# Optimization experiments

Measured on AMD Instinct MI355X. Metric: run time of the kernel, lower is better.

## Reference

```python
import jax, jax.numpy as jnp
import numpy as np

B, S, HID = 1, 4096, 2048
NH, NKV, HD = 8, 4, 256
SCALING = 256.0 ** -0.5
SOFT_CAP = 50.0
WINDOW = 4096
ROPE_THETA = 10000.0
NEG = jnp.finfo(jnp.float32).min


def _build_mask():
    q = np.arange(S)[:, None]
    k = np.arange(S)[None, :]
    causal = k <= q
    windowed = (q - k) < WINDOW
    allowed = causal & windowed
    m = np.where(allowed, 0.0, np.finfo(np.float32).min).astype(np.float32)
    return jnp.asarray(m)[None, None]  # [1,1,S,S]


def setup_inputs() -> dict:
    key = jax.random.key(0)
    ks = jax.random.split(key, 5)
    scale = 0.02
    return {
        "hidden_states": jax.random.normal(ks[0], (B, S, HID), jnp.float32),
        "attention_mask": _build_mask(),
        "position_ids": jnp.arange(S, dtype=jnp.int64)[None, :],
        "wq": jax.random.normal(ks[1], (HID, NH * HD), jnp.float32) * scale,
        "wk": jax.random.normal(ks[2], (HID, NKV * HD), jnp.float32) * scale,
        "wv": jax.random.normal(ks[3], (HID, NKV * HD), jnp.float32) * scale,
        "wo": jax.random.normal(ks[4], (NH * HD, HID), jnp.float32) * scale,
    }


def _rope(position_ids):
    inv_freq = 1.0 / (ROPE_THETA ** (jnp.arange(0, HD, 2, dtype=jnp.float32) / HD))
    freqs = position_ids.astype(jnp.float32)[:, :, None] * inv_freq[None, None, :]  # [B,S,HD/2]
    emb = jnp.concatenate([freqs, freqs], axis=-1)  # [B,S,HD]
    return jnp.cos(emb), jnp.sin(emb)


def _rotate_half(x):
    x1, x2 = x[..., : HD // 2], x[..., HD // 2 :]
    return jnp.concatenate([-x2, x1], axis=-1)


def _attn(hidden_states, attention_mask, position_ids, wq, wk, wv, wo):
    bsz, q_len, _ = hidden_states.shape
    q = (hidden_states @ wq).reshape(bsz, q_len, NH, HD).transpose(0, 2, 1, 3)    # [B,NH,S,HD]
    k = (hidden_states @ wk).reshape(bsz, q_len, NKV, HD).transpose(0, 2, 1, 3)   # [B,NKV,S,HD]
    v = (hidden_states @ wv).reshape(bsz, q_len, NKV, HD).transpose(0, 2, 1, 3)
    cos, sin = _rope(position_ids)
    cos, sin = cos[:, None], sin[:, None]  # [B,1,S,HD]
    q = q * cos + _rotate_half(q) * sin
    k = k * cos + _rotate_half(k) * sin
    n_rep = NH // NKV
    k = jnp.repeat(k, n_rep, axis=1)  # [B,NH,S,HD]
    v = jnp.repeat(v, n_rep, axis=1)
    scores = jnp.einsum("bhqd,bhkd->bhqk", q, k) * SCALING
    scores = jnp.tanh(scores / SOFT_CAP) * SOFT_CAP
    scores = scores + attention_mask
    probs = jax.nn.softmax(scores.astype(jnp.float32), axis=-1).astype(q.dtype)
    out = jnp.einsum("bhqk,bhkd->bhqd", probs, v)  # [B,NH,S,HD]
    out = out.transpose(0, 2, 1, 3).reshape(bsz, q_len, NH * HD)
    return out @ wo


def reference(hidden_states, attention_mask, position_ids, wq, wk, wv, wo):
    return _attn(hidden_states, attention_mask, position_ids, wq, wk, wv, wo)
```

## Files before the change

### kernel.cpp

```cpp
#include <hip/hip_runtime.h>


#define SEQ 4096
#define HIDDEN 2048
#define NHEADS 8
#define HDIM 256

typedef unsigned short u16;
typedef __attribute__((ext_vector_type(8))) __bf16 bf16x8;
typedef __attribute__((ext_vector_type(4))) float f32x4;
typedef __attribute__((ext_vector_type(16))) float f32x16;

static __device__ inline u16 f2bf(float f) {
  union { float f; unsigned u; } x; x.f = f;
  unsigned r = x.u + 0x7FFFu + ((x.u >> 16) & 1u);
  return (u16)(r >> 16);
}
static __device__ inline float bf2f(u16 u) {
  union { unsigned u; float f; } x; x.u = ((unsigned)u) << 16;
  return x.f;
}

typedef __attribute__((address_space(1))) const unsigned int* gp_t;
typedef __attribute__((address_space(3))) unsigned int* lp_t;
static __device__ inline void load_lds16(const u16* g, u16* l) {
  __builtin_amdgcn_global_load_lds((gp_t)g, (lp_t)l, 16, 0, 0);
}


__global__ void convert_hs_kernel(const float* __restrict__ src, u16* __restrict__ dst) {
  int i = blockIdx.x * 256 + threadIdx.x;
  float4 v = ((const float4*)src)[i];
  ushort4 o;
  o.x = f2bf(v.x); o.y = f2bf(v.y); o.z = f2bf(v.z); o.w = f2bf(v.w);
  ((ushort4*)dst)[i] = o;
}

__global__ void transpose_w_kernel(const float* __restrict__ src, u16* __restrict__ dst,
                                   int K, int N) {
  __shared__ u16 tile[64][65];
  int n0 = blockIdx.x * 64, k0 = blockIdx.y * 64;
  int tid = threadIdx.x;
  for (int i = 0; i < 16; i++) {
    int idx = i * 256 + tid; int r = idx >> 6, c = idx & 63;
    tile[r][c] = f2bf(src[(size_t)(k0 + r) * N + n0 + c]);
  }
  __syncthreads();
  for (int i = 0; i < 16; i++) {
    int idx = i * 256 + tid; int r = idx >> 6, c = idx & 63;
    dst[(size_t)(n0 + r) * K + k0 + c] = tile[c][r];
  }
}

__global__ void rope_kernel(u16* qkv) {
  int idx = blockIdx.x * 256 + threadIdx.x;
  int s = idx / (12 * 128);
  int rem = idx - s * (12 * 128);
  int head = rem >> 7;
  int i = rem & 127;
  float inv = __expf(-(float)i * 0.0719557841560639f);
  float ang = (float)s * inv;
  float sn, cs;
  sincosf(ang, &sn, &cs);
  size_t base = (size_t)s * 4096 + head * 256 + i;
  float a = bf2f(qkv[base]);
  float b = bf2f(qkv[base + 128]);
  qkv[base]       = f2bf(a * cs - b * sn);
  qkv[base + 128] = f2bf(b * cs + a * sn);
}

__global__ void transpose_v_kernel(const u16* __restrict__ qkv, u16* __restrict__ vT) {
  __shared__ u16 tile[64][65];
  int d0 = blockIdx.x * 64, s0 = blockIdx.y * 64;
  int tid = threadIdx.x;
  for (int i = 0; i < 16; i++) {
    int idx = i * 256 + tid; int r = idx >> 6, c = idx & 63;
    tile[r][c] = qkv[(size_t)(s0 + r) * 4096 + 3072 + d0 + c];
  }
  __syncthreads();
  for (int i = 0; i < 16; i++) {
    int idx = i * 256 + tid; int r = idx >> 6, c = idx & 63;
    vT[(size_t)(d0 + r) * 4096 + s0 + c] = tile[c][r];
  }
}


template <bool OUT_F32>
__global__ __launch_bounds__(256, 2) void gemm_bf16_kernel(
    const u16* __restrict__ A, const u16* __restrict__ Bt, void* __restrict__ Cout,
    int M, int N, int K) {
  __shared__ __attribute__((aligned(16))) u16 As[128 * 64];
  __shared__ __attribute__((aligned(16))) u16 Bs[128 * 64];
  int tid = threadIdx.x;
  int wave = tid >> 6, lane = tid & 63;
  int lm = lane & 15, qd = lane >> 4;
  int m0 = blockIdx.y * 128, n0 = blockIdx.x * 128;
  int wm = (wave >> 1) * 64, wn = (wave & 1) * 64;

  f32x4 acc[4][4];
#pragma unroll
  for (int a = 0; a < 4; a++)
#pragma unroll
    for (int b = 0; b < 4; b++) acc[a][b] = (f32x4){0.f, 0.f, 0.f, 0.f};

  int srow = lane >> 3;
  int scol = (lane & 7) * 8;

  for (int kt = 0; kt < K; kt += 64) {
    __syncthreads();
#pragma unroll
    for (int t = 0; t < 4; t++) {
      int j = wave * 4 + t;
      int row = j * 8 + srow;
      load_lds16(A  + (size_t)(m0 + row) * K + kt + scol, As + j * 512);
      load_lds16(Bt + (size_t)(n0 + row) * K + kt + scol, Bs + j * 512);
    }
    __syncthreads();
#pragma unroll
    for (int kk = 0; kk < 2; kk++) {
      bf16x8 af[4], bfr[4];
#pragma unroll
      for (int mi = 0; mi < 4; mi++)
        af[mi] = *(const bf16x8*)&As[(wm + mi * 16 + lm) * 64 + kk * 32 + qd * 8];
#pragma unroll
      for (int ni = 0; ni < 4; ni++)
        bfr[ni] = *(const bf16x8*)&Bs[(wn + ni * 16 + lm) * 64 + kk * 32 + qd * 8];
#pragma unroll
      for (int mi = 0; mi < 4; mi++)
#pragma unroll
        for (int ni = 0; ni < 4; ni++)
          acc[mi][ni] = __builtin_amdgcn_mfma_f32_16x16x32_bf16(af[mi], bfr[ni],
                                                               acc[mi][ni], 0, 0, 0);
    }
  }
#pragma unroll
  for (int mi = 0; mi < 4; mi++) {
    int row = m0 + wm + mi * 16 + qd * 4;
#pragma unroll
    for (int ni = 0; ni < 4; ni++) {
      int col = n0 + wn + ni * 16 + lm;
#pragma unroll
      for (int r = 0; r < 4; r++) {
        float v = acc[mi][ni][r];
        if (OUT_F32) ((float*)Cout)[(size_t)(row + r) * N + col] = v;
        else         ((u16*)Cout)[(size_t)(row + r) * N + col] = f2bf(v);
      }
    }
  }
}


__global__ __launch_bounds__(256, 1) void flash_kernel(
    const u16* __restrict__ qkv, const u16* __restrict__ vT,
    u16* __restrict__ attn) {
  __shared__ __attribute__((aligned(16))) u16 Ks[2][64 * 256];
  __shared__ __attribute__((aligned(16))) u16 Vs[2][256 * 64];
  __shared__ __attribute__((aligned(16))) u16 Pl[64 * 64];

  int tid = threadIdx.x;
  int w = tid >> 6, lane = tid & 63;
  int l31 = lane & 31, hi = lane >> 5;
  int qhalf = w >> 1, kh = w & 1, dhalf = w & 1;

  int b = blockIdx.x;
  int h = b & 7;
  int pi = b >> 3;
  int kvh = h >> 1;

  int vlc = (lane & 7) ^ ((lane >> 3) & 7);
  int vro = lane >> 3;

  const u16* Kg  = qkv + 2048 + (size_t)kvh * 256;
  const u16* Vg0 = vT + (size_t)(kvh * 256) * 4096;

  bf16x8 ones;
#pragma unroll
  for (int e = 0; e < 8; e++) ones[e] = (__bf16)1.0f;

  for (int seg = 0; seg < 2; seg++) {
    int qt = seg ? (63 - pi) : pi;
    int T = qt + 1;
    int qs = qt * 64 + qhalf * 32;

    __syncthreads();
    {
      const u16* Qg = qkv + (size_t)(qt * 64) * 4096 + h * 256;
#pragma unroll
      for (int s = 0; s < 8; s++) {
        int kr = (w * 8 + s) * 2 + hi;
        int klc = l31 ^ (kr & 31);
        load_lds16(Qg + (size_t)kr * 4096 + klc * 8, &Ks[0][(w * 8 + s) * 512]);
      }
#pragma unroll
      for (int s = 0; s < 8; s++) {
        int kr = (w * 8 + s) * 2 + hi;
        int klc = l31 ^ (kr & 31);
        load_lds16(Kg + (size_t)kr * 4096 + klc * 8, &Ks[1][(w * 8 + s) * 512]);
        int vr = (w * 8 + s) * 8 + vro;
        load_lds16(Vg0 + (size_t)vr * 4096 + vlc * 8, &Vs[1][(w * 8 + s) * 512]);
      }
    }
    __syncthreads();

    bf16x8 aq[16];
#pragma unroll
    for (int kc = 0; kc < 16; kc++)
      aq[kc] = *(const bf16x8*)&Ks[0][(qhalf * 32 + l31) * 256 +
                                      (((kc * 2 + hi) ^ l31) << 3)];

    __syncthreads();

    f32x16 ao[4];
#pragma unroll
    for (int g = 0; g < 4; g++) ao[g] = (f32x16)(0.f);
    f32x16 al = (f32x16)(0.f);

    for (int t = 0; t < T; t++) {
      int cur = 1 - (t & 1);
      if (t > 0) __syncthreads();

      if (t + 1 < T) {
        int nb = 1 - cur;
        const u16* Kt = Kg + (size_t)((t + 1) * 64) * 4096;
        const u16* Vt = Vg0 + (t + 1) * 64;
#pragma unroll
        for (int s = 0; s < 8; s++) {
          int kr = (w * 8 + s) * 2 + hi;
          int klc = l31 ^ (kr & 31);
          load_lds16(Kt + (size_t)kr * 4096 + klc * 8, &Ks[nb][(w * 8 + s) * 512]);
          int vr = (w * 8 + s) * 8 + vro;
          load_lds16(Vt + (size_t)vr * 4096 + vlc * 8, &Vs[nb][(w * 8 + s) * 512]);
        }
      }

      f32x16 se = (f32x16)(0.f);
      f32x16 so = (f32x16)(0.f);
#pragma unroll
      for (int kc = 0; kc < 8; kc++) {
        bf16x8 bk0 = *(const bf16x8*)&Ks[cur][(kh * 32 + l31) * 256 +
                                              ((((2 * kc) * 2 + hi) ^ l31) << 3)];
        se = __builtin_amdgcn_mfma_f32_32x32x16_bf16(aq[2 * kc], bk0, se, 0, 0, 0);
        bf16x8 bk1 = *(const bf16x8*)&Ks[cur][(kh * 32 + l31) * 256 +
                                              ((((2 * kc + 1) * 2 + hi) ^ l31) << 3)];
        so = __builtin_amdgcn_mfma_f32_32x32x16_bf16(aq[2 * kc + 1], bk1, so, 0, 0, 0);
      }
      f32x16 sacc = se + so;

      bool diag = (t == T - 1);
#pragma unroll
      for (int reg = 0; reg < 16; reg++) {
        int qa = 4 * hi + 8 * (reg >> 2) + (reg & 3);
        int q64 = qhalf * 32 + qa;
        int key64 = kh * 32 + l31;
        float x = sacc[reg] * 0.00125f;
        float x2 = x * x;
        float th = x * (1.f + x2 * (-0.33333333f + x2 * 0.13333333f));
        float p = exp2f(72.134752f * (th - 1.f));
        if (diag && key64 > q64) p = 0.f;
        Pl[q64 * 64 + (((key64 >> 3) ^ (q64 & 7)) << 3) + (key64 & 7)] = f2bf(p);
      }
      asm volatile("s_waitcnt lgkmcnt(0)" ::: "memory");
      __builtin_amdgcn_s_barrier();
      asm volatile("" ::: "memory");

      bf16x8 ap[4];
#pragma unroll
      for (int kc = 0; kc < 4; kc++)
        ap[kc] = *(const bf16x8*)&Pl[(qhalf * 32 + l31) * 64 +
                                     (((kc * 2 + hi) ^ (l31 & 7)) << 3)];
#pragma unroll
      for (int g = 0; g < 4; g++) {
        int dd = dhalf * 128 + g * 32 + l31;
#pragma unroll
        for (int kc = 0; kc < 4; kc++) {
          bf16x8 bv = *(const bf16x8*)&Vs[cur][dd * 64 +
                                              (((kc * 2 + hi) ^ (l31 & 7)) << 3)];
          ao[g] = __builtin_amdgcn_mfma_f32_32x32x16_bf16(ap[kc], bv, ao[g], 0, 0, 0);
        }
      }
#pragma unroll
      for (int kc = 0; kc < 4; kc++)
        al = __builtin_amdgcn_mfma_f32_32x32x16_bf16(ap[kc], ones, al, 0, 0, 0);
    }

    float inv_l[16];
#pragma unroll
    for (int reg = 0; reg < 16; reg++) inv_l[reg] = 1.f / al[reg];
#pragma unroll
    for (int g = 0; g < 4; g++) {
      int col = h * 256 + dhalf * 128 + g * 32 + l31;
#pragma unroll
      for (int reg = 0; reg < 16; reg++) {
        int row = qs + 4 * hi + 8 * (reg >> 2) + (reg & 3);
        attn[(size_t)row * 2048 + col] = f2bf(ao[g][reg] * inv_l[reg]);
      }
    }
  }
}


extern "C" void kernel_launch(void* const* d_in, const int* in_sizes, int n_in,
                              void* d_out, int out_size, void* d_ws, size_t ws_size,
                              hipStream_t stream) {
  const float* hs = (const float*)d_in[0];
  const float* wq = (const float*)d_in[3];
  const float* wk = (const float*)d_in[4];
  const float* wv = (const float*)d_in[5];
  const float* wo = (const float*)d_in[6];
  float* out = (float*)d_out;

  char* ws = (char*)d_ws;
  u16* hsb    = (u16*)(ws);
  u16* wqkvT  = (u16*)(ws + 16777216);
  u16* woT    = (u16*)(ws + 33554432);
  u16* qkv    = (u16*)(ws + 41943040);
  u16* vT     = (u16*)(ws + 75497472);
  u16* attn   = (u16*)(ws + 83886080);

  convert_hs_kernel<<<8192, 256, 0, stream>>>(hs, hsb);
  transpose_w_kernel<<<dim3(32, 32), 256, 0, stream>>>(wq, wqkvT, HIDDEN, 2048);
  transpose_w_kernel<<<dim3(16, 32), 256, 0, stream>>>(wk, wqkvT + (size_t)2048 * HIDDEN, HIDDEN, 1024);
  transpose_w_kernel<<<dim3(16, 32), 256, 0, stream>>>(wv, wqkvT + (size_t)3072 * HIDDEN, HIDDEN, 1024);
  transpose_w_kernel<<<dim3(32, 32), 256, 0, stream>>>(wo, woT, HIDDEN, 2048);

  gemm_bf16_kernel<false><<<dim3(32, 32), 256, 0, stream>>>(hsb, wqkvT, qkv, 4096, 4096, 2048);
  rope_kernel<<<24576, 256, 0, stream>>>(qkv);
  transpose_v_kernel<<<dim3(16, 64), 256, 0, stream>>>(qkv, vT);

  flash_kernel<<<256, 256, 0, stream>>>(qkv, vT, attn);
  gemm_bf16_kernel<true><<<dim3(16, 32), 256, 0, stream>>>(attn, woT, out, 4096, 2048, 2048);
}
```

Baseline: 497.1 us.

## Split flash blocks per query tile and single-buffer K/V to raise occupancy

The flash kernel now launches one block per (head, query tile) instead of pairing two tiles per block, doubling the grid to 512 blocks. K/V LDS buffers go from double to single buffering, roughly halving LDS use so two blocks can share a CU, and launch bounds now request 2 blocks per CU. This trades intra-block prefetch overlap for inter-block overlap via occupancy. Load balance across blocks gets worse because causal tiles differ in length and are no longer paired, and the loop adds a barrier per iteration.

```diff
diff --git a/kernel.cpp b/kernel.cpp
--- a/kernel.cpp
+++ b/kernel.cpp
@@ -150,11 +150,11 @@
 }
 
 
-__global__ __launch_bounds__(256, 1) void flash_kernel(
+__global__ __launch_bounds__(256, 2) void flash_kernel(
     const u16* __restrict__ qkv, const u16* __restrict__ vT,
     u16* __restrict__ attn) {
-  __shared__ __attribute__((aligned(16))) u16 Ks[2][64 * 256];
-  __shared__ __attribute__((aligned(16))) u16 Vs[2][256 * 64];
+  __shared__ __attribute__((aligned(16))) u16 Ks[64 * 256];
+  __shared__ __attribute__((aligned(16))) u16 Vs[256 * 64];
   __shared__ __attribute__((aligned(16))) u16 Pl[64 * 64];
 
   int tid = threadIdx.x;
@@ -163,9 +163,13 @@
   int qhalf = w >> 1, kh = w & 1, dhalf = w & 1;
 
   int b = blockIdx.x;
-  int h = b & 7;
-  int pi = b >> 3;
+  int r = b & 255;
+  int h = r & 7;
+  int pi = r >> 3;
+  int qt = (b >> 8) ? (63 - pi) : pi;
   int kvh = h >> 1;
+  int T = qt + 1;
+  int qs = qt * 64 + qhalf * 32;
 
   int vlc = (lane & 7) ^ ((lane >> 3) & 7);
   int vro = lane >> 3;
@@ -177,123 +181,104 @@
 #pragma unroll
   for (int e = 0; e < 8; e++) ones[e] = (__bf16)1.0f;
 
-  for (int seg = 0; seg < 2; seg++) {
-    int qt = seg ? (63 - pi) : pi;
-    int T = qt + 1;
-    int qs = qt * 64 + qhalf * 32;
-
-    __syncthreads();
+  {
+    const u16* Qg = qkv + (size_t)(qt * 64) * 4096 + h * 256;
+#pragma unroll
+    for (int s = 0; s < 8; s++) {
+      int kr = (w * 8 + s) * 2 + hi;
+      int klc = l31 ^ (kr & 31);
+      load_lds16(Qg + (size_t)kr * 4096 + klc * 8, &Ks[(w * 8 + s) * 512]);
+    }
+  }
+  __syncthreads();
+
+  bf16x8 aq[16];
+#pragma unroll
+  for (int kc = 0; kc < 16; kc++)
+    aq[kc] = *(const bf16x8*)&Ks[(qhalf * 32 + l31) * 256 +
+                                 (((kc * 2 + hi) ^ l31) << 3)];
+  __syncthreads();
+
+  f32x16 ao[4];
+#pragma unroll
+  for (int g = 0; g < 4; g++) ao[g] = (f32x16)(0.f);
+  f32x16 al = (f32x16)(0.f);
+
+  for (int t = 0; t < T; t++) {
     {
-      const u16* Qg = qkv + (size_t)(qt * 64) * 4096 + h * 256;
+      const u16* Kt = Kg + (size_t)(t * 64) * 4096;
+      const u16* Vt = Vg0 + t * 64;
 #pragma unroll
       for (int s = 0; s < 8; s++) {
         int kr = (w * 8 + s) * 2 + hi;
         int klc = l31 ^ (kr & 31);
-        load_lds16(Qg + (size_t)kr * 4096 + klc * 8, &Ks[0][(w * 8 + s) * 512]);
+        load_lds16(Kt + (size_t)kr * 4096 + klc * 8, &Ks[(w * 8 + s) * 512]);
+        int vr = (w * 8 + s) * 8 + vro;
+        load_lds16(Vt + (size_t)vr * 4096 + vlc * 8, &Vs[(w * 8 + s) * 512]);
       }
-#pragma unroll
-      for (int s = 0; s < 8; s++) {
-        int kr = (w * 8 + s) * 2 + hi;
-        int klc = l31 ^ (kr & 31);
-        load_lds16(Kg + (size_t)kr * 4096 + klc * 8, &Ks[1][(w * 8 + s) * 512]);
-        int vr = (w * 8 + s) * 8 + vro;
-        load_lds16(Vg0 + (size_t)vr * 4096 + vlc * 8, &Vs[1][(w * 8 + s) * 512]);
+    }
+    __syncthreads();
+
+    f32x16 se = (f32x16)(0.f);
+    f32x16 so = (f32x16)(0.f);
+#pragma unroll
+    for (int kc = 0; kc < 8; kc++) {
+      bf16x8 bk0 = *(const bf16x8*)&Ks[(kh * 32 + l31) * 256 +
+                                       ((((2 * kc) * 2 + hi) ^ l31) << 3)];
+      se = __builtin_amdgcn_mfma_f32_32x32x16_bf16(aq[2 * kc], bk0, se, 0, 0, 0);
+      bf16x8 bk1 = *(const bf16x8*)&Ks[(kh * 32 + l31) * 256 +
+                                       ((((2 * kc + 1) * 2 + hi) ^ l31) << 3)];
+      so = __builtin_amdgcn_mfma_f32_32x32x16_bf16(aq[2 * kc + 1], bk1, so, 0, 0, 0);
+    }
+    f32x16 sacc = se + so;
+
+    bool diag = (t == T - 1);
+#pragma unroll
+    for (int reg = 0; reg < 16; reg++) {
+      int qa = 4 * hi + 8 * (reg >> 2) + (reg & 3);
+      int q64 = qhalf * 32 + qa;
+      int key64 = kh * 32 + l31;
+      float x = sacc[reg] * 0.00125f;
+      float x2 = x * x;
+      float th = x * (1.f + x2 * (-0.33333333f + x2 * 0.13333333f));
+      float p = exp2f(72.134752f * (th - 1.f));
+      if (diag && key64 > q64) p = 0.f;
+      Pl[q64 * 64 + (((key64 >> 3) ^ (q64 & 7)) << 3) + (key64 & 7)] = f2bf(p);
+    }
+    __syncthreads();
+
+    bf16x8 ap[4];
+#pragma unroll
+    for (int kc = 0; kc < 4; kc++)
+      ap[kc] = *(const bf16x8*)&Pl[(qhalf * 32 + l31) * 64 +
+                                   (((kc * 2 + hi) ^ (l31 & 7)) << 3)];
+#pragma unroll
+    for (int g = 0; g < 4; g++) {
+      int dd = dhalf * 128 + g * 32 + l31;
+#pragma unroll
+      for (int kc = 0; kc < 4; kc++) {
+        bf16x8 bv = *(const bf16x8*)&Vs[dd * 64 +
+                                        (((kc * 2 + hi) ^ (l31 & 7)) << 3)];
+        ao[g] = __builtin_amdgcn_mfma_f32_32x32x16_bf16(ap[kc], bv, ao[g], 0, 0, 0);
       }
     }
-    __syncthreads();
-
-    bf16x8 aq[16];
-#pragma unroll
-    for (int kc = 0; kc < 16; kc++)
-      aq[kc] = *(const bf16x8*)&Ks[0][(qhalf * 32 + l31) * 256 +
-                                      (((kc * 2 + hi) ^ l31) << 3)];
-
-    __syncthreads();
-
-    f32x16 ao[4];
-#pragma unroll
-    for (int g = 0; g < 4; g++) ao[g] = (f32x16)(0.f);
-    f32x16 al = (f32x16)(0.f);
-
-    for (int t = 0; t < T; t++) {
-      int cur = 1 - (t & 1);
-      if (t > 0) __syncthreads();
-
-      if (t + 1 < T) {
-        int nb = 1 - cur;
-        const u16* Kt = Kg + (size_t)((t + 1) * 64) * 4096;
-        const u16* Vt = Vg0 + (t + 1) * 64;
-#pragma unroll
-        for (int s = 0; s < 8; s++) {
-          int kr = (w * 8 + s) * 2 + hi;
-          int klc = l31 ^ (kr & 31);
-          load_lds16(Kt + (size_t)kr * 4096 + klc * 8, &Ks[nb][(w * 8 + s) * 512]);
-          int vr = (w * 8 + s) * 8 + vro;
-          load_lds16(Vt + (size_t)vr * 4096 + vlc * 8, &Vs[nb][(w * 8 + s) * 512]);
-        }
-      }
-
-      f32x16 se = (f32x16)(0.f);
-      f32x16 so = (f32x16)(0.f);
-#pragma unroll
-      for (int kc = 0; kc < 8; kc++) {
-        bf16x8 bk0 = *(const bf16x8*)&Ks[cur][(kh * 32 + l31) * 256 +
-                                              ((((2 * kc) * 2 + hi) ^ l31) << 3)];
-        se = __builtin_amdgcn_mfma_f32_32x32x16_bf16(aq[2 * kc], bk0, se, 0, 0, 0);
-        bf16x8 bk1 = *(const bf16x8*)&Ks[cur][(kh * 32 + l31) * 256 +
-                                              ((((2 * kc + 1) * 2 + hi) ^ l31) << 3)];
-        so = __builtin_amdgcn_mfma_f32_32x32x16_bf16(aq[2 * kc + 1], bk1, so, 0, 0, 0);
-      }
-      f32x16 sacc = se + so;
-
-      bool diag = (t == T - 1);
-#pragma unroll
-      for (int reg = 0; reg < 16; reg++) {
-        int qa = 4 * hi + 8 * (reg >> 2) + (reg & 3);
-        int q64 = qhalf * 32 + qa;
-        int key64 = kh * 32 + l31;
-        float x = sacc[reg] * 0.00125f;
-        float x2 = x * x;
-        float th = x * (1.f + x2 * (-0.33333333f + x2 * 0.13333333f));
-        float p = exp2f(72.134752f * (th - 1.f));
-        if (diag && key64 > q64) p = 0.f;
-        Pl[q64 * 64 + (((key64 >> 3) ^ (q64 & 7)) << 3) + (key64 & 7)] = f2bf(p);
-      }
-      asm volatile("s_waitcnt lgkmcnt(0)" ::: "memory");
-      __builtin_amdgcn_s_barrier();
-      asm volatile("" ::: "memory");
-
-      bf16x8 ap[4];
-#pragma unroll
-      for (int kc = 0; kc < 4; kc++)
-        ap[kc] = *(const bf16x8*)&Pl[(qhalf * 32 + l31) * 64 +
-                                     (((kc * 2 + hi) ^ (l31 & 7)) << 3)];
-#pragma unroll
-      for (int g = 0; g < 4; g++) {
-        int dd = dhalf * 128 + g * 32 + l31;
-#pragma unroll
-        for (int kc = 0; kc < 4; kc++) {
-          bf16x8 bv = *(const bf16x8*)&Vs[cur][dd * 64 +
-                                              (((kc * 2 + hi) ^ (l31 & 7)) << 3)];
-          ao[g] = __builtin_amdgcn_mfma_f32_32x32x16_bf16(ap[kc], bv, ao[g], 0, 0, 0);
-        }
-      }
-#pragma unroll
-      for (int kc = 0; kc < 4; kc++)
-        al = __builtin_amdgcn_mfma_f32_32x32x16_bf16(ap[kc], ones, al, 0, 0, 0);
-    }
-
-    float inv_l[16];
-#pragma unroll
-    for (int reg = 0; reg < 16; reg++) inv_l[reg] = 1.f / al[reg];
-#pragma unroll
-    for (int g = 0; g < 4; g++) {
-      int col = h * 256 + dhalf * 128 + g * 32 + l31;
-#pragma unroll
-      for (int reg = 0; reg < 16; reg++) {
-        int row = qs + 4 * hi + 8 * (reg >> 2) + (reg & 3);
-        attn[(size_t)row * 2048 + col] = f2bf(ao[g][reg] * inv_l[reg]);
-      }
+#pragma unroll
+    for (int kc = 0; kc < 4; kc++)
+      al = __builtin_amdgcn_mfma_f32_32x32x16_bf16(ap[kc], ones, al, 0, 0, 0);
+
+    __syncthreads();
+  }
+
+  float inv_l[16];
+#pragma unroll
+  for (int reg = 0; reg < 16; reg++) inv_l[reg] = 1.f / al[reg];
+#pragma unroll
+  for (int g = 0; g < 4; g++) {
+    int col = h * 256 + dhalf * 128 + g * 32 + l31;
+#pragma unroll
+    for (int reg = 0; reg < 16; reg++) {
+      int row = qs + 4 * hi + 8 * (reg >> 2) + (reg & 3);
+      attn[(size_t)row * 2048 + col] = f2bf(ao[g][reg] * inv_l[reg]);
     }
   }
 }
@@ -327,6 +312,6 @@
   rope_kernel<<<24576, 256, 0, stream>>>(qkv);
   transpose_v_kernel<<<dim3(16, 64), 256, 0, stream>>>(qkv, vT);
 
-  flash_kernel<<<256, 256, 0, stream>>>(qkv, vT, attn);
+  flash_kernel<<<512, 256, 0, stream>>>(qkv, vT, attn);
   gemm_bf16_kernel<true><<<dim3(16, 32), 256, 0, stream>>>(attn, woT, out, 4096, 2048, 2048);
 }
```

Measured after the change: 506.9 us. No clear change (+2.0%).
